# Performance work log

Hardware: AMD Instinct MI355X
Metric: run time of the kernel (lower is better)

## Reference

```python
import jax, jax.numpy as jnp
from jax import lax
import numpy as np

SIGMA = 0.05  # perturbation std (module default)


def setup_inputs() -> dict:
    key = jax.random.key(0)
    k1, k2, k3 = jax.random.split(key, 3)
    return {
        "scores": jax.random.normal(k1, (8, 32, 32), dtype=jnp.float32),      # scorer output (b, h_score, w_score)
        "x_high": jax.random.normal(k2, (8, 3, 1024, 1024), dtype=jnp.float32),
        "noise": jax.random.normal(k3, (8, 500, 1024), dtype=jnp.float32),    # (b, num_samples, d)
        "k": 16,
        "patch_size": 64,
    }


def reference(scores, x_high, noise, k, patch_size):
    b, hs, ws = scores.shape
    _, c, H, W = x_high.shape
    d = hs * ws
    n = noise.shape[1]
    p = patch_size

    # --- min-max normalize scores (as in DPS.forward) ---
    s = scores.reshape(b, d)
    smin = s.min(axis=-1, keepdims=True)
    smax = s.max(axis=-1, keepdims=True)
    s = (s - smin) / (smax - smin + 1e-5)

    # --- PerturbedTopK forward: mean of one-hot top-k over noise samples ---
    perturbed = s[:, None, :] + noise * SIGMA            # (b, n, d)
    _, idx = lax.top_k(perturbed, k)                     # (b, n, k)
    idx = jnp.sort(idx, axis=-1)
    bi = jnp.arange(b)[:, None, None]
    ki = jnp.arange(k)[None, None, :]
    # scatter-count == one_hot(idx, d).mean(axis=1) without materializing (b,n,k,d)
    indicators = jnp.zeros((b, k, d), s.dtype).at[bi, ki, idx].add(1.0 / n)
    indicators = indicators.reshape(b, k, hs, ws)

    # --- pad high-res image exactly like DPS.__init__ ---
    sh, sw = H // hs, W // ws                            # scale_h, scale_w
    top = (p - sh) // 2
    left = (p - sw) // 2
    padded_h = sh * hs + p - 1
    padded_w = sw * ws + p - 1
    x_pad = jnp.pad(x_high, ((0, 0), (0, 0), (top, padded_h - top - H), (left, padded_w - left - W)))
    # only the first (hs-1)*sh + p rows/cols are ever sliced by the loop
    Eh = (hs - 1) * sh + p
    Ew = (ws - 1) * sw + p
    x_pad = x_pad[:, :, :Eh, :Ew]

    # --- weighted patch gather: sum_{i,j} ind[b,k,i,j] * x_pad[b,c, i*sh+u, j*sw+v]
    # expressed as a dilated-kernel cross-correlation, vmapped over batch.
    def per_b(xp, w):  # xp: (c, Eh, Ew), w: (k, hs, ws)
        out = lax.conv_general_dilated(
            xp[:, None],            # lhs (c, 1, Eh, Ew): channels act as batch
            w[:, None],             # rhs (k, 1, hs, ws)
            window_strides=(1, 1),
            padding="VALID",
            rhs_dilation=(sh, sw),
        )                           # (c, k, p, p)
        return out.transpose(1, 0, 2, 3)  # (k, c, p, p)

    patches = jax.vmap(per_b)(x_pad, indicators)  # (b, k, c, p, p)
    return patches
```

## Files before the change

### kernel.cpp

```cpp
#include <hip/hip_runtime.h>

constexpr int NB = 8;
constexpr int ND = 1024;
constexpr int NS = 500;
constexpr int NK = 16;
constexpr int NC = 3;
constexpr int NH = 1024;
constexpr int NW = 1024;
constexpr int NP = 64;
constexpr int PTOP = 16;
constexpr int PLEFT = 16;
constexpr float SIGMA = 0.05f;

__global__ void normalize_kernel(const float* __restrict__ scores,
                                 float* __restrict__ s_norm,
                                 int* __restrict__ counts) {
    int blk = blockIdx.x;
    int t = threadIdx.x;

    int4 z4 = make_int4(0, 0, 0, 0);
    ((int4*)counts)[blk * 512 + t] = z4;
    ((int4*)counts)[blk * 512 + 256 + t] = z4;

    if (blk >= NB) return;
    int b = blk;
    float v[4];
#pragma unroll
    for (int q = 0; q < 4; q++) v[q] = scores[b * ND + t + 256 * q];
    float mn = fminf(fminf(v[0], v[1]), fminf(v[2], v[3]));
    float mx = fmaxf(fmaxf(v[0], v[1]), fmaxf(v[2], v[3]));
#pragma unroll
    for (int off = 1; off < 64; off <<= 1) {
        mn = fminf(mn, __shfl_xor(mn, off));
        mx = fmaxf(mx, __shfl_xor(mx, off));
    }
    __shared__ float smn[4], smx[4];
    int wave = t >> 6, lane = t & 63;
    if (lane == 0) { smn[wave] = mn; smx[wave] = mx; }
    __syncthreads();
    mn = fminf(fminf(smn[0], smn[1]), fminf(smn[2], smn[3]));
    mx = fmaxf(fmaxf(smx[0], smx[1]), fmaxf(smx[2], smx[3]));
    float den = mx - mn + 1e-5f;
#pragma unroll
    for (int q = 0; q < 4; q++)
        s_norm[b * ND + t + 256 * q] = (v[q] - mn) / den;
}

__global__ void topk_kernel(const float* __restrict__ s_norm,
                            const float* __restrict__ noise,
                            int* __restrict__ counts) {
    int t = threadIdx.x;
    int wave = t >> 6, lane = t & 63;
    int sid = blockIdx.x * 4 + wave;
    int b = sid / NS;

    const float* sp = s_norm + b * ND;
    const float* npp = noise + (size_t)sid * ND;

    float v[16];
#pragma unroll
    for (int q = 0; q < 16; q++) {
        int j = q * 64 + lane;
        v[q] = sp[j] + npp[j] * SIGMA;
    }

    int myj = 0x7fffffff;
    for (int it = 0; it < NK; it++) {
        float bv = v[0];
        int bq = 0;
#pragma unroll
        for (int q = 1; q < 16; q++)
            if (v[q] > bv) { bv = v[q]; bq = q; }
        int bj = bq * 64 + lane;
#pragma unroll
        for (int off = 1; off < 64; off <<= 1) {
            float ov = __shfl_xor(bv, off);
            int oj = __shfl_xor(bj, off);
            if (ov > bv || (ov == bv && oj < bj)) { bv = ov; bj = oj; }
        }
        if (lane == it) myj = bj;
        int wq = bj >> 6, wl = bj & 63;
#pragma unroll
        for (int q = 0; q < 16; q++)
            v[q] = (q == wq && lane == wl) ? -1e30f : v[q];
    }

    int rank = 0;
#pragma unroll
    for (int u = 0; u < NK; u++) {
        int other = __shfl(myj, u);
        rank += (other < myj) ? 1 : 0;
    }
    if (lane < NK)
        atomicAdd(&counts[(b * NK + rank) * ND + myj], 1);
}

__global__ void union_kernel(const int* __restrict__ counts,
                             int* __restrict__ ucell,
                             float* __restrict__ uw,
                             int* __restrict__ nunion) {
    int b = blockIdx.x;
    int t = threadIdx.x;
    int lane = t & 63, wave = t >> 6;
    const int* cp = counts + b * NK * ND;

    unsigned nz = 0;
    for (int kk = 0; kk < NK; kk++) {
        int4 c4 = *(const int4*)(cp + kk * ND + t * 4);
        if (c4.x) nz |= 1;
        if (c4.y) nz |= 2;
        if (c4.z) nz |= 4;
        if (c4.w) nz |= 8;
    }
    int cnt = __popc(nz);
    int incl = cnt;
#pragma unroll
    for (int off = 1; off < 64; off <<= 1) {
        int o = __shfl_up(incl, off);
        if (lane >= off) incl += o;
    }
    int excl = incl - cnt;
    __shared__ int wtot[4];
    if (lane == 63) wtot[wave] = incl;
    __syncthreads();
    int base = 0;
    for (int w = 0; w < wave; w++) base += wtot[w];
    int pos = base + excl;

    const float invn = 1.0f / (float)NS;
    int* up = ucell + b * ND;
    float* wp = uw + (size_t)b * ND * NK;
#pragma unroll
    for (int q = 0; q < 4; q++) {
        if (nz & (1u << q)) {
            int cell = t * 4 + q;
            int i = cell >> 5, j = cell & 31;
            int ent = (i << 15) | (j << 5) |
                      ((i == 0) ? 1 : 0) | ((i == 31) ? 2 : 0) |
                      ((j == 0) ? 4 : 0) | ((j == 31) ? 8 : 0);
            up[pos] = ent;
            for (int kk = 0; kk < NK; kk++)
                wp[(size_t)pos * NK + kk] = (float)cp[kk * ND + cell] * invn;
            pos++;
        }
    }
    if (t == 0) nunion[b] = wtot[0] + wtot[1] + wtot[2] + wtot[3];
}

constexpr int EC = 16;
__global__ void gather_kernel(const int* __restrict__ ucell,
                              const float* __restrict__ uw,
                              const int* __restrict__ nunion,
                              const float* __restrict__ x_high,
                              float* __restrict__ out) {
    int blk = blockIdx.x;
    int bc = blk % 24;
    int ii = blk / 24;
    int gg = ii & 15;
    int kq = ii >> 4;
    int b = bc / 3, c = bc % 3;
    int t = threadIdx.x;
    int x = t & 63;
    int y = gg * 4 + (t >> 6);

    int m = nunion[b];

    __shared__ int lc[ND];
    __shared__ float lw[ND][8];

    for (int i = t; i < m; i += 256) {
        lc[i] = ucell[b * ND + i];
        const float4* wsrc =
            (const float4*)(uw + (size_t)(b * ND + i) * NK + kq * 8);
        float4 w0 = wsrc[0], w1 = wsrc[1];
        *(float4*)&lw[i][0] = w0;
        *(float4*)&lw[i][4] = w1;
    }
    __syncthreads();

    const float* xp = x_high + (size_t)bc * (NH * NW);
    int ym = y - PTOP;
    int xm = x - PLEFT;
    int off = ym * NW + xm;
    int mask = ((ym < 0) ? 1 : 0) | ((ym >= 32) ? 2 : 0) |
               ((xm < 0) ? 4 : 0) | ((xm >= 32) ? 8 : 0);

    float acc[8];
#pragma unroll
    for (int q = 0; q < 8; q++) acc[q] = 0.f;

    for (int base = 0; base < m; base += EC) {
        float vv[EC];
#pragma unroll
        for (int j = 0; j < EC; j++) {
            int ee = base + j;
            int ent = lc[ee < m ? ee : 0];
            bool ok = (ee < m) && ((ent & mask) == 0);
            int idx = ok ? ((ent & ~15) + off) : 0;
            float v = xp[idx];
            vv[j] = ok ? v : 0.f;
        }
#pragma unroll
        for (int j = 0; j < EC; j++) {
            int ee = base + j;
            int es = ee < m ? ee : 0;
            float4 wa = *(const float4*)&lw[es][0];
            float4 wb = *(const float4*)&lw[es][4];
            float v = vv[j];
            acc[0] += wa.x * v; acc[1] += wa.y * v;
            acc[2] += wa.z * v; acc[3] += wa.w * v;
            acc[4] += wb.x * v; acc[5] += wb.y * v;
            acc[6] += wb.z * v; acc[7] += wb.w * v;
        }
    }

#pragma unroll
    for (int q = 0; q < 8; q++) {
        int kk = kq * 8 + q;
        int o = ((b * NK + kk) * NC + c) * (NP * NP) + y * NP + x;
        out[o] = acc[q];
    }
}

extern "C" void kernel_launch(void* const* d_in, const int* in_sizes, int n_in,
                              void* d_out, int out_size, void* d_ws, size_t ws_size,
                              hipStream_t stream) {
    const float* scores = (const float*)d_in[0];
    const float* x_high = (const float*)d_in[1];
    const float* noise  = (const float*)d_in[2];

    char* ws = (char*)d_ws;
    float* s_norm = (float*)ws;
    int* counts   = (int*)(ws + 32 * 1024);
    int* ucell    = (int*)(ws + 544 * 1024);
    float* uw     = (float*)(ws + 576 * 1024);
    int* nunion   = (int*)(ws + 1088 * 1024);

    normalize_kernel<<<64, 256, 0, stream>>>(scores, s_norm, counts);
    topk_kernel<<<NB * NS / 4, 256, 0, stream>>>(s_norm, noise, counts);
    union_kernel<<<NB, 256, 0, stream>>>(counts, ucell, uw, nunion);
    gather_kernel<<<24 * 32, 256, 0, stream>>>(ucell, uw, nunion, x_high,
                                               (float*)d_out);
}
```

Baseline: 57.57 us.

## Vectorize gather with float4 pixel loads and split union entries across lanes

Each wave now covers a patch row with 16 lanes loading four consecutive pixels as float4, and the four lane groups take interleaved union entries. Partial sums are combined with cross-lane shuffles, and each lane writes two float4 outputs. Shared memory is capped at 768 entries, and any entries beyond that are handled by a slow fallback loop that reads global memory. The aim is fewer memory instructions per pixel and higher arithmetic intensity, at the cost of a shuffle reduction and more accumulator registers.

```diff
diff --git a/kernel.cpp b/kernel.cpp
--- a/kernel.cpp
+++ b/kernel.cpp
@@ -147,7 +147,7 @@
     if (t == 0) nunion[b] = wtot[0] + wtot[1] + wtot[2] + wtot[3];
 }
 
-constexpr int EC = 16;
+constexpr int MAXE = 768;
 __global__ void gather_kernel(const int* __restrict__ ucell,
                               const float* __restrict__ uw,
                               const int* __restrict__ nunion,
@@ -160,15 +160,19 @@
     int kq = ii >> 4;
     int b = bc / 3, c = bc % 3;
     int t = threadIdx.x;
-    int x = t & 63;
-    int y = gg * 4 + (t >> 6);
+    int w = t >> 6;
+    int lane = t & 63;
+    int e4 = lane >> 4;
+    int c4 = lane & 15;
+    int y = gg * 4 + w;
 
     int m = nunion[b];
-
-    __shared__ int lc[ND];
-    __shared__ float lw[ND][8];
-
-    for (int i = t; i < m; i += 256) {
+    int mc = m < MAXE ? m : MAXE;
+
+    __shared__ int lc[MAXE];
+    __shared__ float lw[MAXE][8];
+
+    for (int i = t; i < mc; i += 256) {
         lc[i] = ucell[b * ND + i];
         const float4* wsrc =
             (const float4*)(uw + (size_t)(b * ND + i) * NK + kq * 8);
@@ -180,46 +184,85 @@
 
     const float* xp = x_high + (size_t)bc * (NH * NW);
     int ym = y - PTOP;
-    int xm = x - PLEFT;
+    int xm = 4 * c4 - PLEFT;
     int off = ym * NW + xm;
     int mask = ((ym < 0) ? 1 : 0) | ((ym >= 32) ? 2 : 0) |
                ((xm < 0) ? 4 : 0) | ((xm >= 32) ? 8 : 0);
 
-    float acc[8];
-#pragma unroll
-    for (int q = 0; q < 8; q++) acc[q] = 0.f;
-
-    for (int base = 0; base < m; base += EC) {
-        float vv[EC];
-#pragma unroll
-        for (int j = 0; j < EC; j++) {
-            int ee = base + j;
-            int ent = lc[ee < m ? ee : 0];
-            bool ok = (ee < m) && ((ent & mask) == 0);
+    float4 acc4[8];
+#pragma unroll
+    for (int q = 0; q < 8; q++) acc4[q] = make_float4(0.f, 0.f, 0.f, 0.f);
+
+    for (int base = 0; base < mc; base += 16) {
+        float4 vv[4];
+        int es[4];
+#pragma unroll
+        for (int j = 0; j < 4; j++) {
+            int ee = base + j * 4 + e4;
+            bool in = (ee < mc);
+            int e = in ? ee : 0;
+            es[j] = e;
+            int ent = lc[e];
+            bool ok = in && ((ent & mask) == 0);
             int idx = ok ? ((ent & ~15) + off) : 0;
-            float v = xp[idx];
-            vv[j] = ok ? v : 0.f;
-        }
-#pragma unroll
-        for (int j = 0; j < EC; j++) {
-            int ee = base + j;
-            int es = ee < m ? ee : 0;
-            float4 wa = *(const float4*)&lw[es][0];
-            float4 wb = *(const float4*)&lw[es][4];
-            float v = vv[j];
-            acc[0] += wa.x * v; acc[1] += wa.y * v;
-            acc[2] += wa.z * v; acc[3] += wa.w * v;
-            acc[4] += wb.x * v; acc[5] += wb.y * v;
-            acc[6] += wb.z * v; acc[7] += wb.w * v;
+            float4 v = *(const float4*)(xp + idx);
+            vv[j].x = ok ? v.x : 0.f;
+            vv[j].y = ok ? v.y : 0.f;
+            vv[j].z = ok ? v.z : 0.f;
+            vv[j].w = ok ? v.w : 0.f;
+        }
+#pragma unroll
+        for (int j = 0; j < 4; j++) {
+            float4 w0 = *(const float4*)&lw[es[j]][0];
+            float4 w1 = *(const float4*)&lw[es[j]][4];
+            float4 v = vv[j];
+            acc4[0].x += w0.x * v.x; acc4[0].y += w0.x * v.y; acc4[0].z += w0.x * v.z; acc4[0].w += w0.x * v.w;
+            acc4[1].x += w0.y * v.x; acc4[1].y += w0.y * v.y; acc4[1].z += w0.y * v.z; acc4[1].w += w0.y * v.w;
+            acc4[2].x += w0.z * v.x; acc4[2].y += w0.z * v.y; acc4[2].z += w0.z * v.z; acc4[2].w += w0.z * v.w;
+            acc4[3].x += w0.w * v.x; acc4[3].y += w0.w * v.y; acc4[3].z += w0.w * v.z; acc4[3].w += w0.w * v.w;
+            acc4[4].x += w1.x * v.x; acc4[4].y += w1.x * v.y; acc4[4].z += w1.x * v.z; acc4[4].w += w1.x * v.w;
+            acc4[5].x += w1.y * v.x; acc4[5].y += w1.y * v.y; acc4[5].z += w1.y * v.z; acc4[5].w += w1.y * v.w;
+            acc4[6].x += w1.z * v.x; acc4[6].y += w1.z * v.y; acc4[6].z += w1.z * v.z; acc4[6].w += w1.z * v.w;
+            acc4[7].x += w1.w * v.x; acc4[7].y += w1.w * v.y; acc4[7].z += w1.w * v.z; acc4[7].w += w1.w * v.w;
+        }
+    }
+
+    for (int e = MAXE; e < m; e++) {
+        int ent = ucell[b * ND + e];
+        bool ok = ((ent & mask) == 0);
+        int idx = ok ? ((ent & ~15) + off) : 0;
+        float4 v = *(const float4*)(xp + idx);
+        if (!ok) v = make_float4(0.f, 0.f, 0.f, 0.f);
+        const float* wq = uw + (size_t)(b * ND + e) * NK + kq * 8;
+        if (e4 == 0) {
+#pragma unroll
+            for (int q = 0; q < 8; q++) {
+                float wv = wq[q];
+                acc4[q].x += wv * v.x; acc4[q].y += wv * v.y;
+                acc4[q].z += wv * v.z; acc4[q].w += wv * v.w;
+            }
         }
     }
 
 #pragma unroll
     for (int q = 0; q < 8; q++) {
-        int kk = kq * 8 + q;
-        int o = ((b * NK + kk) * NC + c) * (NP * NP) + y * NP + x;
-        out[o] = acc[q];
-    }
+        acc4[q].x += __shfl_xor(acc4[q].x, 16);
+        acc4[q].y += __shfl_xor(acc4[q].y, 16);
+        acc4[q].z += __shfl_xor(acc4[q].z, 16);
+        acc4[q].w += __shfl_xor(acc4[q].w, 16);
+        acc4[q].x += __shfl_xor(acc4[q].x, 32);
+        acc4[q].y += __shfl_xor(acc4[q].y, 32);
+        acc4[q].z += __shfl_xor(acc4[q].z, 32);
+        acc4[q].w += __shfl_xor(acc4[q].w, 32);
+    }
+
+    float4 r0 = (e4 == 0) ? acc4[0] : (e4 == 1) ? acc4[2] : (e4 == 2) ? acc4[4] : acc4[6];
+    float4 r1 = (e4 == 0) ? acc4[1] : (e4 == 1) ? acc4[3] : (e4 == 2) ? acc4[5] : acc4[7];
+    int kk0 = kq * 8 + e4 * 2;
+    size_t o0 = ((size_t)(b * NK + kk0) * NC + c) * (NP * NP) + y * NP + 4 * c4;
+    size_t o1 = ((size_t)(b * NK + kk0 + 1) * NC + c) * (NP * NP) + y * NP + 4 * c4;
+    *(float4*)(out + o0) = r0;
+    *(float4*)(out + o1) = r1;
 }
 
 extern "C" void kernel_launch(void* const* d_in, const int* in_sizes, int n_in,
```

Result: slower. 64.89 us (+12.7%).

## Split union entries across waves per output row and reduce in shared memory

Applied to the files above, without the earlier changes.

The gather kernel now gives each block a single output row and spreads the union cell list across its four waves. Each wave accumulates a partial sum and the partials are combined through shared memory. The grid grows fourfold, and weights and cell entries are read directly from global memory instead of being staged in LDS, with launch bounds set for higher occupancy. The intent is more parallelism and shorter serial loops per thread, at the cost of a block-level reduction and repeated global or cache reads of the weights.

```diff
diff --git a/kernel.cpp b/kernel.cpp
--- a/kernel.cpp
+++ b/kernel.cpp
@@ -147,38 +147,27 @@
     if (t == 0) nunion[b] = wtot[0] + wtot[1] + wtot[2] + wtot[3];
 }
 
-constexpr int EC = 16;
-__global__ void gather_kernel(const int* __restrict__ ucell,
-                              const float* __restrict__ uw,
-                              const int* __restrict__ nunion,
-                              const float* __restrict__ x_high,
-                              float* __restrict__ out) {
+__global__ void __launch_bounds__(256, 8)
+gather_kernel(const int* __restrict__ ucell,
+              const float* __restrict__ uw,
+              const int* __restrict__ nunion,
+              const float* __restrict__ x_high,
+              float* __restrict__ out) {
     int blk = blockIdx.x;
     int bc = blk % 24;
     int ii = blk / 24;
-    int gg = ii & 15;
-    int kq = ii >> 4;
+    int y  = ii & 63;
+    int kq = ii >> 6;
     int b = bc / 3, c = bc % 3;
     int t = threadIdx.x;
+    int w = t >> 6;
     int x = t & 63;
-    int y = gg * 4 + (t >> 6);
-
-    int m = nunion[b];
-
-    __shared__ int lc[ND];
-    __shared__ float lw[ND][8];
-
-    for (int i = t; i < m; i += 256) {
-        lc[i] = ucell[b * ND + i];
-        const float4* wsrc =
-            (const float4*)(uw + (size_t)(b * ND + i) * NK + kq * 8);
-        float4 w0 = wsrc[0], w1 = wsrc[1];
-        *(float4*)&lw[i][0] = w0;
-        *(float4*)&lw[i][4] = w1;
-    }
-    __syncthreads();
-
+
+    int U = nunion[b];
+    const int* up = ucell + b * ND;
+    const float* wp = uw + (size_t)b * ND * NK + kq * 8;
     const float* xp = x_high + (size_t)bc * (NH * NW);
+
     int ym = y - PTOP;
     int xm = x - PLEFT;
     int off = ym * NW + xm;
@@ -189,36 +178,46 @@
 #pragma unroll
     for (int q = 0; q < 8; q++) acc[q] = 0.f;
 
-    for (int base = 0; base < m; base += EC) {
-        float vv[EC];
-#pragma unroll
-        for (int j = 0; j < EC; j++) {
-            int ee = base + j;
-            int ent = lc[ee < m ? ee : 0];
-            bool ok = (ee < m) && ((ent & mask) == 0);
+    for (int e0 = w; e0 < U; e0 += 16) {
+        float vv[4];
+        int es[4];
+#pragma unroll
+        for (int j = 0; j < 4; j++) {
+            int e = e0 + 4 * j;
+            bool in = (e < U);
+            int ee = in ? e : 0;
+            es[j] = ee;
+            int ent = up[ee];
+            bool ok = in && ((ent & mask) == 0);
             int idx = ok ? ((ent & ~15) + off) : 0;
             float v = xp[idx];
             vv[j] = ok ? v : 0.f;
         }
 #pragma unroll
-        for (int j = 0; j < EC; j++) {
-            int ee = base + j;
-            int es = ee < m ? ee : 0;
-            float4 wa = *(const float4*)&lw[es][0];
-            float4 wb = *(const float4*)&lw[es][4];
+        for (int j = 0; j < 4; j++) {
+            const float4* wq = (const float4*)(wp + (size_t)es[j] * NK);
+            float4 w0 = wq[0], w1 = wq[1];
             float v = vv[j];
-            acc[0] += wa.x * v; acc[1] += wa.y * v;
-            acc[2] += wa.z * v; acc[3] += wa.w * v;
-            acc[4] += wb.x * v; acc[5] += wb.y * v;
-            acc[6] += wb.z * v; acc[7] += wb.w * v;
-        }
-    }
-
-#pragma unroll
-    for (int q = 0; q < 8; q++) {
-        int kk = kq * 8 + q;
-        int o = ((b * NK + kk) * NC + c) * (NP * NP) + y * NP + x;
-        out[o] = acc[q];
+            acc[0] += w0.x * v; acc[1] += w0.y * v;
+            acc[2] += w0.z * v; acc[3] += w0.w * v;
+            acc[4] += w1.x * v; acc[5] += w1.y * v;
+            acc[6] += w1.z * v; acc[7] += w1.w * v;
+        }
+    }
+
+    __shared__ float red[3][64][9];
+    if (w > 0) {
+#pragma unroll
+        for (int q = 0; q < 8; q++) red[w - 1][x][q] = acc[q];
+    }
+    __syncthreads();
+    if (w == 0) {
+#pragma unroll
+        for (int q = 0; q < 8; q++) {
+            float s = acc[q] + red[0][x][q] + red[1][x][q] + red[2][x][q];
+            int kk = kq * 8 + q;
+            out[((size_t)(b * NK + kk) * NC + c) * (NP * NP) + y * NP + x] = s;
+        }
     }
 }
 
@@ -239,6 +238,6 @@
     normalize_kernel<<<64, 256, 0, stream>>>(scores, s_norm, counts);
     topk_kernel<<<NB * NS / 4, 256, 0, stream>>>(s_norm, noise, counts);
     union_kernel<<<NB, 256, 0, stream>>>(counts, ucell, uw, nunion);
-    gather_kernel<<<24 * 32, 256, 0, stream>>>(ucell, uw, nunion, x_high,
-                                               (float*)d_out);
-}
+    gather_kernel<<<24 * 128, 256, 0, stream>>>(ucell, uw, nunion, x_high,
+                                                (float*)d_out);
+}
```

After: 71.95 us. +25.0%, slower.
